# Kernel optimization log

Measured on AMD Instinct MI355X. Metric: run time of the kernel, lower is better.

Reference implementation:

```python
import jax, jax.numpy as jnp
import numpy as np

HEADS = 8
BLOCK = 32

def setup_inputs() -> dict:
    key = jax.random.key(0)
    ks = jax.random.split(key, 4)
    b, n, d, f = 4, 4096, 1024, 128
    x = jax.random.normal(ks[0], (b, n, d), dtype=jnp.float32)
    w_qkv = jax.random.normal(ks[1], (3 * d, d), dtype=jnp.float32) * (d ** -0.5)
    w_out = jax.random.normal(ks[2], (d, d), dtype=jnp.float32) * (d ** -0.5)
    b_out = jnp.zeros((d,), dtype=jnp.float32)
    proj = jax.random.normal(ks[3], (HEADS, d // HEADS, f), dtype=jnp.float32) * ((d // HEADS) ** -0.5)
    return {"x": x, "w_qkv": w_qkv, "w_out": w_out, "b_out": b_out, "proj": proj}

def reference(x, w_qkv, w_out, b_out, proj):
    b, n, d = x.shape
    h = HEADS
    hd = d // h
    nb = n // BLOCK
    # QKV projection (torch Linear: x @ W.T)
    qkv = x @ w_qkv.T  # (b, n, 3d)
    q, k, v = jnp.split(qkv, 3, axis=-1)
    def to_blocks(t):
        # (b, n, d) -> (b, h, nb, BLOCK, hd)
        return t.reshape(b, n, h, hd).transpose(0, 2, 1, 3).reshape(b, h, nb, BLOCK, hd)
    q, k, v = to_blocks(q), to_blocks(k), to_blocks(v)
    # per-head feature map: elu(x @ proj) + 1
    qp = jax.nn.elu(jnp.einsum('bhcsd,hdf->bhcsf', q, proj)) + 1.0
    kp = jax.nn.elu(jnp.einsum('bhcsd,hdf->bhcsf', k, proj)) + 1.0
    # per-block kv state and normalizer
    kv = jnp.einsum('bhcsf,bhcsd->bhcfd', kp, v)          # (b,h,nb,f,hd)
    num = jnp.einsum('bhcsf,bhcfd->bhcsd', qp, kv)        # (b,h,nb,BLOCK,hd)
    ksum = kp.sum(axis=3)                                 # (b,h,nb,f)
    z = 1.0 / (jnp.einsum('bhcsf,bhcf->bhcs', qp, ksum) + 1e-8)
    out = num * z[..., None]
    # merge blocks and heads: (b,h,nb,BLOCK,hd) -> (b,n,d)
    out = out.reshape(b, h, n, hd).transpose(0, 2, 1, 3).reshape(b, n, d)
    # output projection (dropout inert in eval)
    return out @ w_out.T + b_out
```

## Files before the change

### kernel.cpp

```cpp
#include <hip/hip_runtime.h>
#include <hip/hip_bf16.h>
#include <stdint.h>
#include <stddef.h>

typedef __bf16 bf16_t;
typedef __bf16 bf16x8 __attribute__((ext_vector_type(8)));
typedef __bf16 bf16x4 __attribute__((ext_vector_type(4)));
typedef float  f32x4  __attribute__((ext_vector_type(4)));

static __device__ __forceinline__ f32x4 mfma16x16x32(bf16x8 a, bf16x8 b, f32x4 c) {
  return __builtin_amdgcn_mfma_f32_16x16x32_bf16(a, b, c, 0, 0, 0);
}

static __device__ __forceinline__ void gld_lds16(const void* g, void* l) {
  __builtin_amdgcn_global_load_lds(
      (const __attribute__((address_space(1))) unsigned int*)g,
      (__attribute__((address_space(3))) unsigned int*)l, 16, 0, 0);
}

#define BARW()   __builtin_amdgcn_s_barrier()
#define SCHED0() __builtin_amdgcn_sched_barrier(0)
#define LGKM0()  asm volatile("s_waitcnt lgkmcnt(0)" ::: "memory")
#define LGKMN(n) asm volatile("s_waitcnt lgkmcnt(" #n ")" ::: "memory")
#define VMCNT(n) asm volatile("s_waitcnt vmcnt(" #n ")" ::: "memory")
#define PRIO(p)  __builtin_amdgcn_s_setprio(p)

__global__ __launch_bounds__(256) void prep(const float* __restrict__ wqkv,
                                            const float* __restrict__ proj,
                                            const float* __restrict__ wout,
                                            const float* __restrict__ x,
                                            bf16_t* __restrict__ B1t2,
                                            bf16_t* __restrict__ Wv,
                                            bf16_t* __restrict__ W3t,
                                            bf16_t* __restrict__ xbf) {
  const int b = blockIdx.x;
  const int tid = threadIdx.x;
  if (b >= 1536) {
    for (int i = (b - 1536) * 256 + tid; i < 4194304; i += 262144) {
      float4 v = *(const float4*)(x + (size_t)i * 4);
      bf16x4 o;
      o[0] = (bf16_t)v.x; o[1] = (bf16_t)v.y; o[2] = (bf16_t)v.z; o[3] = (bf16_t)v.w;
      *(bf16x4*)(xbf + (size_t)i * 4) = o;
    }
    return;
  }
  if (b >= 1024) {
    const float* src = (b < 1280) ? wout : (wqkv + (size_t)2048 * 1024);
    bf16_t* dst = (b < 1280) ? W3t : Wv;
    size_t off = ((size_t)((b - 1024) & 255) * 4096) + tid * 16;
#pragma unroll
    for (int it = 0; it < 4; ++it) {
      float4 v = *(const float4*)(src + off + it * 4);
      bf16x4 o;
      o[0] = (bf16_t)v.x; o[1] = (bf16_t)v.y; o[2] = (bf16_t)v.z; o[3] = (bf16_t)v.w;
      *(bf16x4*)(dst + off + it * 4) = o;
    }
    return;
  }
  const int combo = b >> 6;
  const int kt    = (b >> 2) & 15;
  const int fq    = b & 3;
  const int qk    = combo >> 3;
  const int h     = combo & 7;
  const int klocal = tid & 63;
  const int fg     = tid >> 6;
  const int k      = kt * 64 + klocal;

  const float* wbase = wqkv + ((size_t)(qk * 1024 + h * 128)) * 1024 + k;
  const float* pbase = proj + (size_t)h * 16384 + fq * 32 + fg * 8;

  float acc[8];
#pragma unroll
  for (int i = 0; i < 8; ++i) acc[i] = 0.f;

  for (int c = 0; c < 128; ++c) {
    float a = wbase[(size_t)c * 1024];
    const float4* p = (const float4*)(pbase + (size_t)c * 128);
    float4 p0 = p[0], p1 = p[1];
    acc[0] += a * p0.x; acc[1] += a * p0.y; acc[2] += a * p0.z; acc[3] += a * p0.w;
    acc[4] += a * p1.x; acc[5] += a * p1.y; acc[6] += a * p1.z; acc[7] += a * p1.w;
  }
  bf16_t* obase = B1t2 + ((size_t)(h * 256 + qk * 128 + fq * 32 + fg * 8)) * 1024 + k;
#pragma unroll
  for (int i = 0; i < 8; ++i) obase[(size_t)i * 1024] = (bf16_t)acc[i];
}

#define GEMM_MAINLOOP_DECLS()                                                  \
  const int tid  = threadIdx.x;                                                \
  const int lane = tid & 63;                                                   \
  const int wid  = tid >> 6;                                                   \
  const int wm   = wid >> 2;                                                   \
  const int wn   = wid & 3;                                                    \
  const int lr   = lane & 15;                                                  \
  const int g0   = lane >> 4;                                                  \
  int srow[2], sgl[2];                                                         \
  _Pragma("unroll")                                                            \
  for (int l = 0; l < 2; ++l) {                                                \
    int idx = l * 512 + tid;                                                   \
    srow[l] = idx >> 3;                                                        \
    sgl[l]  = (idx & 7) ^ (srow[l] & 7);                                       \
  }

#define STAGE_T(arr, base, half, kt, K_)                                       \
  {                                                                            \
    const bf16_t* s_ = (base) + (size_t)((half) * 128) * (K_) + (kt) * 64;     \
    bf16_t* d_ = &(arr)[half][0];                                              \
    _Pragma("unroll")                                                          \
    for (int l_ = 0; l_ < 2; ++l_)                                             \
      gld_lds16(s_ + (size_t)srow[l_] * (K_) + sgl[l_] * 8,                    \
                d_ + (l_ * 512 + tid) * 8);                                    \
  }

#define RD_A(buf, qm)                                                          \
  _Pragma("unroll")                                                            \
  for (int t_ = 0; t_ < 4; ++t_) {                                             \
    int r_ = (qm) * 64 + t_ * 16 + lr;                                         \
    _Pragma("unroll")                                                          \
    for (int kh_ = 0; kh_ < 2; ++kh_) {                                        \
      int gl_ = (g0 + kh_ * 4) ^ (r_ & 7);                                     \
      a[t_][kh_] = *(const bf16x8*)(&sA[buf][wm][r_ * 64 + gl_ * 8]);          \
    }                                                                          \
  }
#define RD_B(buf, qn, breg)                                                    \
  _Pragma("unroll")                                                            \
  for (int u_ = 0; u_ < 2; ++u_) {                                             \
    int r_ = (wn & 1) * 64 + (qn) * 32 + u_ * 16 + lr;                         \
    _Pragma("unroll")                                                          \
    for (int kh_ = 0; kh_ < 2; ++kh_) {                                        \
      int gl_ = (g0 + kh_ * 4) ^ (r_ & 7);                                     \
      breg[u_][kh_] = *(const bf16x8*)(&sB[buf][wn >> 1][r_ * 64 + gl_ * 8]);  \
    }                                                                          \
  }
#define MMA(qm, qn, breg)                                                      \
  _Pragma("unroll")                                                            \
  for (int mi_ = 0; mi_ < 4; ++mi_)                                            \
    _Pragma("unroll")                                                          \
    for (int nj_ = 0; nj_ < 2; ++nj_)                                          \
      _Pragma("unroll")                                                        \
      for (int kh_ = 0; kh_ < 2; ++kh_)                                        \
        acc[(qm) * 4 + mi_][(qn) * 2 + nj_] =                                  \
            mfma16x16x32(a[mi_][kh_], breg[nj_][kh_],                          \
                         acc[(qm) * 4 + mi_][(qn) * 2 + nj_]);

#define GEMM_MAINLOOP_BODY(Abase, Bbase, K_, NT_)                              \
  f32x4 acc[8][4] = {};                                                        \
  bf16x8 a[4][2], b0[2][2], b1[2][2];                                          \
  STAGE_T(sA[0], Abase, 0, 0, K_); STAGE_T(sA[0], Abase, 1, 0, K_);            \
  STAGE_T(sB[0], Bbase, 0, 0, K_); STAGE_T(sB[0], Bbase, 1, 0, K_);            \
  STAGE_T(sA[1], Abase, 0, 1, K_); STAGE_T(sA[1], Abase, 1, 1, K_);            \
  STAGE_T(sB[1], Bbase, 0, 1, K_); STAGE_T(sB[1], Bbase, 1, 1, K_);            \
  VMCNT(8);                                                                    \
  BARW();                                                                      \
  _Pragma("unroll 2")                                                          \
  for (int j = 0; j < (NT_); ++j) {                                            \
    const int cur = j & 1;                                                     \
    const bool pf = (j + 2) < (NT_);                                           \
    RD_A(cur, 0);                                                              \
    RD_B(cur, 0, b0);                                                          \
    SCHED0(); LGKMN(8); BARW(); LGKM0(); SCHED0();                             \
    PRIO(1); MMA(0, 0, b0); PRIO(0);                                           \
    SCHED0(); BARW();                                                          \
    RD_B(cur, 1, b1);                                                          \
    SCHED0(); BARW(); LGKM0(); SCHED0();                                       \
    PRIO(1); MMA(0, 1, b1); PRIO(0);                                           \
    SCHED0(); BARW();                                                          \
    RD_A(cur, 1);                                                              \
    if (pf) { STAGE_T(sB[cur], Bbase, 0, j + 2, K_); STAGE_T(sB[cur], Bbase, 1, j + 2, K_); } \
    SCHED0(); LGKMN(4); BARW(); LGKM0(); SCHED0();                             \
    PRIO(1); MMA(1, 1, b1); PRIO(0);                                           \
    SCHED0(); BARW();                                                          \
    if (pf) { STAGE_T(sA[cur], Abase, 0, j + 2, K_); STAGE_T(sA[cur], Abase, 1, j + 2, K_); } \
    SCHED0(); BARW();                                                          \
    PRIO(1); MMA(1, 0, b0); PRIO(0);                                           \
    if (pf) { VMCNT(8); } else { VMCNT(0); }                                   \
    SCHED0(); BARW();                                                          \
  }

__global__ __launch_bounds__(512, 2) void gemm256(const bf16_t* __restrict__ A,
                                                  const bf16_t* __restrict__ Bt,
                                                  void* __restrict__ Cout,
                                                  const float* __restrict__ bias,
                                                  int N, int K, int NB) {
  __shared__ __align__(16) bf16_t sA[2][2][8192];
  __shared__ __align__(16) bf16_t sB[2][2][8192];
  GEMM_MAINLOOP_DECLS();

  const int nwg = gridDim.x;
  const int cpx = nwg >> 3;
  const int bid = blockIdx.x;
  const int swz = (bid & 7) * cpx + (bid >> 3);
  const int m0 = (swz / NB) * 256;
  const int n0 = (swz % NB) * 256;
  const int NT = K >> 6;

  const bf16_t* Abase = A  + (size_t)m0 * K;
  const bf16_t* Bbase = Bt + (size_t)n0 * K;

  GEMM_MAINLOOP_BODY(Abase, Bbase, K, NT);

#pragma unroll
  for (int i = 0; i < 8; ++i) {
#pragma unroll
    for (int jn = 0; jn < 4; ++jn) {
      const int n = n0 + wn * 64 + jn * 16 + lr;
#pragma unroll
      for (int r = 0; r < 4; ++r) {
        const int m = m0 + wm * 128 + i * 16 + g0 * 4 + r;
        ((float*)Cout)[(size_t)m * N + n] = acc[i][jn][r] + bias[n];
      }
    }
  }
}

__global__ __launch_bounds__(512, 2) void gemm_fused(const bf16_t* __restrict__ A,
                                                     const bf16_t* __restrict__ Bt,
                                                     const bf16_t* __restrict__ Wv,
                                                     bf16_t* __restrict__ VtG,
                                                     bf16_t* __restrict__ OUT1) {
  __shared__ __align__(16) bf16_t sA[2][2][8192];
  __shared__ __align__(16) bf16_t sB[2][2][8192];
  GEMM_MAINLOOP_DECLS();

  const int nwg = gridDim.x;
  const int cpx = nwg >> 3;
  const int bid = blockIdx.x;
  const int swz = (bid & 7) * cpx + (bid >> 3);
  const int m0 = (swz >> 3) * 256;
  const int h  = swz & 7;
  const int K  = 1024;
  const int NT = 16;

  const bf16_t* Abase = A  + (size_t)m0 * K;
  const bf16_t* Bbase = Bt + (size_t)(h * 256) * K;
  bf16_t* VtGblk = VtG + (size_t)swz * 32768;

  {
    const bf16_t* Wbase = Wv + (size_t)(h * 128) * 1024;
    f32x4 accv[4][4] = {};
    bf16x8 av[4][2], bv[4][2];
    const int wmv = wid >> 1;
    const int wnv = wid & 1;
    const int ah  = wmv >> 1;
    const int ar0 = (wmv & 1) * 64;

    STAGE_T(sA[0], Abase, 0, 0, K); STAGE_T(sA[0], Abase, 1, 0, K);
    STAGE_T(sB[0], Wbase, 0, 0, K);
    STAGE_T(sA[1], Abase, 0, 1, K); STAGE_T(sA[1], Abase, 1, 1, K);
    STAGE_T(sB[1], Wbase, 0, 1, K);
    VMCNT(6);
    BARW();
#pragma unroll 2
    for (int j = 0; j < NT; ++j) {
      const int cur = j & 1;
      const bool pf = (j + 2) < NT;
#pragma unroll
      for (int mi = 0; mi < 4; ++mi) {
        int r_ = ar0 + mi * 16 + lr;
#pragma unroll
        for (int kh = 0; kh < 2; ++kh) {
          int gl = (g0 + kh * 4) ^ (r_ & 7);
          av[mi][kh] = *(const bf16x8*)(&sA[cur][ah][r_ * 64 + gl * 8]);
        }
      }
#pragma unroll
      for (int di = 0; di < 4; ++di) {
        int r_ = wnv * 64 + di * 16 + lr;
#pragma unroll
        for (int kh = 0; kh < 2; ++kh) {
          int gl = (g0 + kh * 4) ^ (r_ & 7);
          bv[di][kh] = *(const bf16x8*)(&sB[cur][0][r_ * 64 + gl * 8]);
        }
      }
      SCHED0(); LGKMN(8); BARW(); LGKM0(); SCHED0();
      PRIO(1);
#pragma unroll
      for (int mi = 0; mi < 4; ++mi)
#pragma unroll
        for (int di = 0; di < 2; ++di)
#pragma unroll
          for (int kh = 0; kh < 2; ++kh)
            accv[mi][di] = mfma16x16x32(av[mi][kh], bv[di][kh], accv[mi][di]);
      PRIO(0);
      if (pf) { STAGE_T(sB[cur], Wbase, 0, j + 2, K); }
      SCHED0(); BARW();
      PRIO(1);
#pragma unroll
      for (int mi = 0; mi < 4; ++mi)
#pragma unroll
        for (int di = 2; di < 4; ++di)
#pragma unroll
          for (int kh = 0; kh < 2; ++kh)
            accv[mi][di] = mfma16x16x32(av[mi][kh], bv[di][kh], accv[mi][di]);
      PRIO(0);
      if (pf) { STAGE_T(sA[cur], Abase, 0, j + 2, K); STAGE_T(sA[cur], Abase, 1, j + 2, K); }
      if (pf) { VMCNT(6); } else { VMCNT(0); }
      SCHED0(); BARW();
    }
#pragma unroll
    for (int mi = 0; mi < 4; ++mi)
#pragma unroll
      for (int di = 0; di < 4; ++di) {
        int d  = wnv * 64 + di * 16 + lr;
        int mb = wmv * 64 + mi * 16 + g0 * 4;
        int c  = mb >> 3;
        int g  = (c & 24) | ((c ^ d) & 7);
        bf16x4 pk;
#pragma unroll
        for (int r = 0; r < 4; ++r) pk[r] = (bf16_t)accv[mi][di][r];
        *(bf16x4*)((char*)VtGblk + d * 512 + g * 16 + (mb & 7) * 2) = pk;
      }
  }

  GEMM_MAINLOOP_BODY(Abase, Bbase, K, NT);

  char* sQb = (char*)(&sA[0][0][0]);
  char* sKb = (char*)(&sB[0][0][0]);

  {
    char* dbase = (wn < 2) ? sQb : sKb;
#pragma unroll
    for (int i = 0; i < 8; ++i)
#pragma unroll
      for (int jn = 0; jn < 4; ++jn)
#pragma unroll
        for (int r = 0; r < 4; ++r) {
          int row = wm * 128 + i * 16 + g0 * 4 + r;
          int col = (wn & 1) * 64 + jn * 16 + lr;
          float v = acc[i][jn][r];
          v = v > 0.f ? v + 1.f : __expf(v);
          int gq = col >> 3;
          int g  = (gq & 8) | ((gq ^ row) & 7);
          *(bf16_t*)(dbase + row * 256 + g * 16 + (col & 7) * 2) = (bf16_t)v;
        }
  }
  LGKM0();
  BARW();

  const int cb = wm * 4 + wn;
  const int rb = cb * 32;
  bf16x8 aS[4][2], bS[4][2];
#pragma unroll
  for (int kh = 0; kh < 4; ++kh) {
#pragma unroll
    for (int t = 0; t < 2; ++t) {
      int row = rb + t * 16 + lr;
      int gq = kh * 4 + g0;
      int g  = (gq & 8) | ((gq ^ row) & 7);
      aS[kh][t] = *(const bf16x8*)(sQb + row * 256 + g * 16);
      bS[kh][t] = *(const bf16x8*)(sKb + row * 256 + g * 16);
    }
  }
  SCHED0(); LGKM0(); BARW();

  {
#pragma unroll
    for (int l = 0; l < 8; ++l) {
      int gd = l * 512 + tid;
      gld_lds16(VtGblk + (size_t)gd * 8, sKb + gd * 16);
    }
  }
  SCHED0();

  f32x4 sacc[2][2] = {};
#pragma unroll
  for (int kh = 0; kh < 4; ++kh)
#pragma unroll
    for (int mt = 0; mt < 2; ++mt)
#pragma unroll
      for (int nt = 0; nt < 2; ++nt)
        sacc[mt][nt] = mfma16x16x32(aS[kh][mt], bS[kh][nt], sacc[mt][nt]);

  float zin[2][4];
#pragma unroll
  for (int mt = 0; mt < 2; ++mt)
#pragma unroll
    for (int r = 0; r < 4; ++r) {
      float s = sacc[mt][0][r] + sacc[mt][1][r];
      s += __shfl_xor(s, 1); s += __shfl_xor(s, 2);
      s += __shfl_xor(s, 4); s += __shfl_xor(s, 8);
      zin[mt][r] = 1.0f / (s + 1e-8f);
    }

  char* Pl = sQb;
#pragma unroll
  for (int mt = 0; mt < 2; ++mt)
#pragma unroll
    for (int nt = 0; nt < 2; ++nt)
#pragma unroll
      for (int r = 0; r < 4; ++r) {
        int i = mt * 16 + g0 * 4 + r;
        int jj = nt * 16 + lr;
        *(bf16_t*)(Pl + cb * 2560 + i * 80 + jj * 2) =
            (bf16_t)(sacc[mt][nt][r] * zin[mt][r]);
      }
  LGKM0();
  VMCNT(0);
  BARW();

  bf16x8 aP[2];
#pragma unroll
  for (int mt = 0; mt < 2; ++mt)
    aP[mt] = *(const bf16x8*)(Pl + cb * 2560 + (mt * 16 + lr) * 80 + g0 * 16);
#pragma unroll
  for (int dt = 0; dt < 8; ++dt) {
    int row = dt * 16 + lr;
    int gidx = cb * 4 + g0;
    int g = (gidx & 24) | ((gidx ^ row) & 7);
    bf16x8 bV = *(const bf16x8*)(sKb + row * 512 + g * 16);
#pragma unroll
    for (int mt = 0; mt < 2; ++mt) {
      f32x4 z = {};
      f32x4 o = mfma16x16x32(aP[mt], bV, z);
#pragma unroll
      for (int r = 0; r < 4; ++r) {
        int m = m0 + rb + mt * 16 + g0 * 4 + r;
        int d = h * 128 + dt * 16 + lr;
        OUT1[(size_t)m * 1024 + d] = (bf16_t)o[r];
      }
    }
  }
}

extern "C" void kernel_launch(void* const* d_in, const int* in_sizes, int n_in,
                              void* d_out, int out_size, void* d_ws, size_t ws_size,
                              hipStream_t stream) {
  const float* x     = (const float*)d_in[0];
  const float* w_qkv = (const float*)d_in[1];
  const float* w_out = (const float*)d_in[2];
  const float* b_out = (const float*)d_in[3];
  const float* proj  = (const float*)d_in[4];
  float* out = (float*)d_out;

  char* ws = (char*)d_ws;
  bf16_t* xbf  = (bf16_t*)(ws);
  bf16_t* B1t2 = (bf16_t*)(ws + 33554432);
  bf16_t* Wv   = (bf16_t*)(ws + 37748736);
  bf16_t* W3t  = (bf16_t*)(ws + 39845888);
  bf16_t* VtG  = (bf16_t*)(ws + 41943040);
  bf16_t* OUT1 = (bf16_t*)(ws + 75497472);

  (void)in_sizes; (void)n_in; (void)out_size; (void)ws_size;

  prep<<<2560, 256, 0, stream>>>(w_qkv, proj, w_out, x, B1t2, Wv, W3t, xbf);
  gemm_fused<<<512, 512, 0, stream>>>(xbf, B1t2, Wv, VtG, OUT1);
  gemm256<<<256, 512, 0, stream>>>(OUT1, W3t, (void*)out, b_out, 1024, 1024, 4);
}
```

Before: 200.0 us.

## Split prep weight-fold blocks finer and drop sched barriers in GEMM loops

The prep kernel's W_qkv×proj folding now uses 2048 blocks, each computing 4 output features per thread instead of 8. This doubles parallelism in that phase, and the grid grows to keep the cast and x-conversion ranges intact. Separately, the sched_barrier(0) fences around the waitcnt/barrier points in the GEMM main loops are removed, letting the compiler reorder instructions across those points. The risk is that the compiler's scheduling breaks the hand-tuned interleaving of LDS reads, MFMAs and global loads.

```diff
diff --git a/kernel.cpp b/kernel.cpp
--- a/kernel.cpp
+++ b/kernel.cpp
@@ -35,8 +35,8 @@
                                             bf16_t* __restrict__ xbf) {
   const int b = blockIdx.x;
   const int tid = threadIdx.x;
-  if (b >= 1536) {
-    for (int i = (b - 1536) * 256 + tid; i < 4194304; i += 262144) {
+  if (b >= 2560) {
+    for (int i = (b - 2560) * 256 + tid; i < 4194304; i += 262144) {
       float4 v = *(const float4*)(x + (size_t)i * 4);
       bf16x4 o;
       o[0] = (bf16_t)v.x; o[1] = (bf16_t)v.y; o[2] = (bf16_t)v.z; o[3] = (bf16_t)v.w;
@@ -44,10 +44,10 @@
     }
     return;
   }
-  if (b >= 1024) {
-    const float* src = (b < 1280) ? wout : (wqkv + (size_t)2048 * 1024);
-    bf16_t* dst = (b < 1280) ? W3t : Wv;
-    size_t off = ((size_t)((b - 1024) & 255) * 4096) + tid * 16;
+  if (b >= 2048) {
+    const float* src = (b < 2304) ? wout : (wqkv + (size_t)2048 * 1024);
+    bf16_t* dst = (b < 2304) ? W3t : Wv;
+    size_t off = ((size_t)((b - 2048) & 255) * 4096) + tid * 16;
 #pragma unroll
     for (int it = 0; it < 4; ++it) {
       float4 v = *(const float4*)(src + off + it * 4);
@@ -57,32 +57,29 @@
     }
     return;
   }
-  const int combo = b >> 6;
-  const int kt    = (b >> 2) & 15;
-  const int fq    = b & 3;
+  const int combo = b >> 7;
+  const int kt    = (b >> 3) & 15;
+  const int fq    = b & 7;
   const int qk    = combo >> 3;
   const int h     = combo & 7;
   const int klocal = tid & 63;
   const int fg     = tid >> 6;
   const int k      = kt * 64 + klocal;
+  const int f0     = fq * 16 + fg * 4;
 
   const float* wbase = wqkv + ((size_t)(qk * 1024 + h * 128)) * 1024 + k;
-  const float* pbase = proj + (size_t)h * 16384 + fq * 32 + fg * 8;
-
-  float acc[8];
-#pragma unroll
-  for (int i = 0; i < 8; ++i) acc[i] = 0.f;
+  const float* pbase = proj + (size_t)h * 16384 + f0;
+
+  float acc[4] = {0.f, 0.f, 0.f, 0.f};
 
   for (int c = 0; c < 128; ++c) {
     float a = wbase[(size_t)c * 1024];
-    const float4* p = (const float4*)(pbase + (size_t)c * 128);
-    float4 p0 = p[0], p1 = p[1];
+    float4 p0 = *(const float4*)(pbase + (size_t)c * 128);
     acc[0] += a * p0.x; acc[1] += a * p0.y; acc[2] += a * p0.z; acc[3] += a * p0.w;
-    acc[4] += a * p1.x; acc[5] += a * p1.y; acc[6] += a * p1.z; acc[7] += a * p1.w;
-  }
-  bf16_t* obase = B1t2 + ((size_t)(h * 256 + qk * 128 + fq * 32 + fg * 8)) * 1024 + k;
-#pragma unroll
-  for (int i = 0; i < 8; ++i) obase[(size_t)i * 1024] = (bf16_t)acc[i];
+  }
+  bf16_t* obase = B1t2 + ((size_t)(h * 256 + qk * 128 + f0)) * 1024 + k;
+#pragma unroll
+  for (int i = 0; i < 4; ++i) obase[(size_t)i * 1024] = (bf16_t)acc[i];
 }
 
 #define GEMM_MAINLOOP_DECLS()                                                  \
@@ -157,23 +154,23 @@
     const bool pf = (j + 2) < (NT_);                                           \
     RD_A(cur, 0);                                                              \
     RD_B(cur, 0, b0);                                                          \
-    SCHED0(); LGKMN(8); BARW(); LGKM0(); SCHED0();                             \
+    LGKMN(8); BARW(); LGKM0();                                                 \
     PRIO(1); MMA(0, 0, b0); PRIO(0);                                           \
-    SCHED0(); BARW();                                                          \
+    BARW();                                                                    \
     RD_B(cur, 1, b1);                                                          \
-    SCHED0(); BARW(); LGKM0(); SCHED0();                                       \
+    BARW(); LGKM0();                                                           \
     PRIO(1); MMA(0, 1, b1); PRIO(0);                                           \
-    SCHED0(); BARW();                                                          \
+    BARW();                                                                    \
     RD_A(cur, 1);                                                              \
     if (pf) { STAGE_T(sB[cur], Bbase, 0, j + 2, K_); STAGE_T(sB[cur], Bbase, 1, j + 2, K_); } \
-    SCHED0(); LGKMN(4); BARW(); LGKM0(); SCHED0();                             \
+    LGKMN(4); BARW(); LGKM0();                                                 \
     PRIO(1); MMA(1, 1, b1); PRIO(0);                                           \
-    SCHED0(); BARW();                                                          \
+    BARW();                                                                    \
     if (pf) { STAGE_T(sA[cur], Abase, 0, j + 2, K_); STAGE_T(sA[cur], Abase, 1, j + 2, K_); } \
-    SCHED0(); BARW();                                                          \
+    BARW();                                                                    \
     PRIO(1); MMA(1, 0, b0); PRIO(0);                                           \
     if (pf) { VMCNT(8); } else { VMCNT(0); }                                   \
-    SCHED0(); BARW();                                                          \
+    BARW();                                                                    \
   }
 
 __global__ __launch_bounds__(512, 2) void gemm256(const bf16_t* __restrict__ A,
@@ -271,7 +268,7 @@
           bv[di][kh] = *(const bf16x8*)(&sB[cur][0][r_ * 64 + gl * 8]);
         }
       }
-      SCHED0(); LGKMN(8); BARW(); LGKM0(); SCHED0();
+      LGKMN(8); BARW(); LGKM0();
       PRIO(1);
 #pragma unroll
       for (int mi = 0; mi < 4; ++mi)
@@ -282,7 +279,7 @@
             accv[mi][di] = mfma16x16x32(av[mi][kh], bv[di][kh], accv[mi][di]);
       PRIO(0);
       if (pf) { STAGE_T(sB[cur], Wbase, 0, j + 2, K); }
-      SCHED0(); BARW();
+      BARW();
       PRIO(1);
 #pragma unroll
       for (int mi = 0; mi < 4; ++mi)
@@ -294,7 +291,7 @@
       PRIO(0);
       if (pf) { STAGE_T(sA[cur], Abase, 0, j + 2, K); STAGE_T(sA[cur], Abase, 1, j + 2, K); }
       if (pf) { VMCNT(6); } else { VMCNT(0); }
-      SCHED0(); BARW();
+      BARW();
     }
 #pragma unroll
     for (int mi = 0; mi < 4; ++mi)
@@ -441,7 +438,7 @@
 
   (void)in_sizes; (void)n_in; (void)out_size; (void)ws_size;
 
-  prep<<<2560, 256, 0, stream>>>(w_qkv, proj, w_out, x, B1t2, Wv, W3t, xbf);
+  prep<<<3584, 256, 0, stream>>>(w_qkv, proj, w_out, x, B1t2, Wv, W3t, xbf);
   gemm_fused<<<512, 512, 0, stream>>>(xbf, B1t2, Wv, VtG, OUT1);
   gemm256<<<256, 512, 0, stream>>>(OUT1, W3t, (void*)out, b_out, 1024, 1024, 4);
 }
```

Measured after the change: 207.7 us. 3.8% more time.
